# Kernel tuning notes

Hardware: AMD Instinct MI355X
Metric: run time of the kernel (lower is better)

The kernel has to match this reference:

```python
import jax, jax.numpy as jnp
import numpy as np

EMB = 512
HEADS = 8
WINDOW = 128


def setup_inputs() -> dict:
    key = jax.random.key(0)
    ks = jax.random.split(key, 9)
    s = 1.0 / np.sqrt(EMB)
    x = jax.random.normal(ks[0], (2, 4096, EMB), dtype=jnp.float32)
    mk = lambda k: jax.random.uniform(k, (EMB, EMB), jnp.float32, -s, s)
    mb = lambda k: jax.random.uniform(k, (EMB,), jnp.float32, -s, s)
    return {
        "x": x,
        "Wq": mk(ks[1]), "bq": mb(ks[2]),
        "Wk": mk(ks[3]), "bk": mb(ks[4]),
        "Wv": mk(ks[5]), "bv": mb(ks[6]),
        "Wo": mk(ks[7]), "bo": mb(ks[8]),
    }


def _split_heads(y, b, n):
    # [b, n, emb] -> [b, h, n, d]
    return y.reshape(b, n, HEADS, EMB // HEADS).transpose(0, 2, 1, 3)


def reference(x, Wq, bq, Wk, bk, Wv, bv, Wo, bo):
    b, n, _ = x.shape
    q = _split_heads(x @ Wq.T + bq, b, n)
    k = _split_heads(x @ Wk.T + bk, b, n)
    v = _split_heads(x @ Wv.T + bv, b, n)
    energy = jnp.einsum('bhqd,bhkd->bhqk', q, k)  # [b,h,n,n]
    idx = jnp.arange(n)
    # banded mask: disallowed where |i - j| > window (matches torch loop)
    disallow = jnp.abs(idx[:, None] - idx[None, :]) > WINDOW
    fmin = jnp.float32(np.finfo(np.float32).min)
    energy = jnp.where(disallow[None, None], fmin, energy)
    att = jax.nn.softmax(energy / jnp.float32(np.sqrt(EMB)), axis=-1)
    out = jnp.einsum('bhql,bhld->bhqd', att, v)
    out = out.transpose(0, 2, 1, 3).reshape(b, n, EMB)
    return out @ Wo.T + bo
```

## Files before the change

### kernel.cpp

```cpp
#include <hip/hip_runtime.h>

#define EMB 512
#define HEADS 8
#define HD 64
#define NSEQ 4096
#define BATCH 2
#define WINDOW 128

typedef unsigned short u16;
typedef __attribute__((ext_vector_type(8))) short bf16x8;
typedef __attribute__((ext_vector_type(4))) float f32x4;

#define GP 40

__device__ __forceinline__ float bf2f(u16 u) {
    union { unsigned int i; float f; } x;
    x.i = ((unsigned int)u) << 16;
    return x.f;
}

__device__ __forceinline__ u16 f2bf(float f) {
    union { float f; unsigned int i; } x;
    x.f = f;
    unsigned int i = x.i;
    unsigned int lsb = (i >> 16) & 1u;
    i += 0x7fffu + lsb;
    return (u16)(i >> 16);
}

struct raw8 { uint4 lo, hi; };

__device__ __forceinline__ raw8 loadraw8(const void* base, size_t off, int isbf) {
    raw8 r;
    if (isbf) {
        r.lo = *(const uint4*)((const u16*)base + off);
    } else {
        const float* f = (const float*)base + off;
        r.lo = *(const uint4*)f;
        r.hi = *(const uint4*)(f + 4);
    }
    return r;
}

__device__ __forceinline__ uint4 cvt8(const raw8& r, int isbf) {
    if (isbf) return r.lo;
    const float* a = (const float*)&r.lo;
    const float* b = (const float*)&r.hi;
    uint4 o;
    o.x = (unsigned)f2bf(a[0]) | ((unsigned)f2bf(a[1]) << 16);
    o.y = (unsigned)f2bf(a[2]) | ((unsigned)f2bf(a[3]) << 16);
    o.z = (unsigned)f2bf(b[0]) | ((unsigned)f2bf(b[1]) << 16);
    o.w = (unsigned)f2bf(b[2]) | ((unsigned)f2bf(b[3]) << 16);
    return o;
}

__device__ __forceinline__ float loadScalar(const void* base, int i, int isbf) {
    return isbf ? bf2f(((const u16*)base)[i]) : ((const float*)base)[i];
}

__device__ __forceinline__ int probe_bf16(const void* p) {
    const int lane = threadIdx.x & 63;
    u16 w = ((const u16*)p)[lane * 2];
    int e = (w >> 7) & 0xff;
    bool sane = (w == 0) || (e >= 100 && e <= 140);
    unsigned long long m = __ballot(sane);
    return __popcll(m) >= 48;
}

__global__ __launch_bounds__(256)
void qkv_gemm(const void* __restrict__ X,
              const void* __restrict__ Wq, const void* __restrict__ bq,
              const void* __restrict__ Wk, const void* __restrict__ bk,
              const void* __restrict__ Wv, const void* __restrict__ bv,
              u16* __restrict__ qo, u16* __restrict__ ko, u16* __restrict__ vo,
              int* __restrict__ flags)
{
    __shared__ __align__(16) u16 As[128 * GP];
    __shared__ __align__(16) u16 Bs[128 * GP];

    const int tid  = threadIdx.x;
    const int wave = tid >> 6;
    const int lane = tid & 63;
    const int quad = lane >> 4;
    const int l16  = lane & 15;
    const int wm = wave >> 1, wn = wave & 1;

    const int m0 = blockIdx.x * 128;
    const int by = blockIdx.y;
    const int wsel = by >> 2;
    const int n0 = (by & 3) * 128;

    const void* W  = (wsel == 0) ? Wq : (wsel == 1) ? Wk : Wv;
    const void* bi = (wsel == 0) ? bq : (wsel == 1) ? bk : bv;
    u16* out       = (wsel == 0) ? qo : (wsel == 1) ? ko : vo;
    const float oscale = (wsel == 0) ? 0.04419417382415922f : 1.0f;

    const int fx = probe_bf16(X);
    const int fw = probe_bf16(W);
    const int fb = probe_bf16(bi);
    if (blockIdx.x == 0 && by == 0 && tid == 0) flags[0] = fx;

    f32x4 acc[4][4];
#pragma unroll
    for (int i = 0; i < 4; ++i)
#pragma unroll
        for (int j = 0; j < 4; ++j)
            acc[i][j] = (f32x4){0.f, 0.f, 0.f, 0.f};

    const int c1 = tid, c2 = tid + 256;
    const int r1 = c1 >> 2, k1 = (c1 & 3) * 8;
    const int r2 = c2 >> 2, k2 = (c2 & 3) * 8;

    raw8 a1 = loadraw8(X, (size_t)(m0 + r1) * EMB + k1, fx);
    raw8 a2 = loadraw8(X, (size_t)(m0 + r2) * EMB + k2, fx);
    raw8 b1 = loadraw8(W, (size_t)(n0 + r1) * EMB + k1, fw);
    raw8 b2 = loadraw8(W, (size_t)(n0 + r2) * EMB + k2, fw);

    for (int kt = 0; kt < 16; ++kt) {
        __syncthreads();
        *(uint4*)&As[r1 * GP + k1] = cvt8(a1, fx);
        *(uint4*)&As[r2 * GP + k2] = cvt8(a2, fx);
        *(uint4*)&Bs[r1 * GP + k1] = cvt8(b1, fw);
        *(uint4*)&Bs[r2 * GP + k2] = cvt8(b2, fw);
        __syncthreads();

        if (kt < 15) {
            const int kk0 = (kt + 1) * 32;
            a1 = loadraw8(X, (size_t)(m0 + r1) * EMB + kk0 + k1, fx);
            a2 = loadraw8(X, (size_t)(m0 + r2) * EMB + kk0 + k2, fx);
            b1 = loadraw8(W, (size_t)(n0 + r1) * EMB + kk0 + k1, fw);
            b2 = loadraw8(W, (size_t)(n0 + r2) * EMB + kk0 + k2, fw);
        }

        bf16x8 af[4], bfr[4];
#pragma unroll
        for (int i = 0; i < 4; ++i)
            af[i] = *(const bf16x8*)&As[(wm * 64 + i * 16 + l16) * GP + quad * 8];
#pragma unroll
        for (int j = 0; j < 4; ++j)
            bfr[j] = *(const bf16x8*)&Bs[(wn * 64 + j * 16 + l16) * GP + quad * 8];
#pragma unroll
        for (int i = 0; i < 4; ++i)
#pragma unroll
            for (int j = 0; j < 4; ++j)
                acc[i][j] = __builtin_amdgcn_mfma_f32_16x16x32_bf16(af[i], bfr[j], acc[i][j], 0, 0, 0);
    }

#pragma unroll
    for (int j = 0; j < 4; ++j) {
        const int col = n0 + wn * 64 + j * 16 + l16;
        const float bv_ = loadScalar(bi, col, fb);
        const int h = col >> 6, d = col & 63;
#pragma unroll
        for (int i = 0; i < 4; ++i) {
#pragma unroll
            for (int r = 0; r < 4; ++r) {
                const int row = m0 + wm * 64 + i * 16 + quad * 4 + r;
                const int b = row >> 12, n = row & 4095;
                out[(((size_t)(b * HEADS + h) * NSEQ) + n) * HD + d] =
                    f2bf((acc[i][j][r] + bv_) * oscale);
            }
        }
    }
}

#define KP 72
__global__ __launch_bounds__(256)
void attn_mfma(const u16* __restrict__ q, const u16* __restrict__ k,
               const u16* __restrict__ v, u16* __restrict__ ao)
{
    __shared__ __align__(16) u16 Ks[64 * KP];
    __shared__ __align__(16) u16 Vt[64 * KP];
    __shared__ __align__(16) u16 Pb[4][16 * KP];

    const int tid  = threadIdx.x;
    const int wave = tid >> 6;
    const int lane = tid & 63;
    const int quad = lane >> 4;
    const int l16  = lane & 15;

    const int bh = blockIdx.y;
    const int q0 = blockIdx.x * 64;
    const int qw = q0 + wave * 16;
    const size_t base = (size_t)bh * NSEQ * HD;

    bf16x8 qa0 = *(const bf16x8*)(q + base + (size_t)(qw + l16) * HD + quad * 8);
    bf16x8 qa1 = *(const bf16x8*)(q + base + (size_t)(qw + l16) * HD + 32 + quad * 8);

    f32x4 O[4];
    float m_run[4], l_run[4];
#pragma unroll
    for (int t = 0; t < 4; ++t) O[t] = (f32x4){0.f, 0.f, 0.f, 0.f};
#pragma unroll
    for (int r = 0; r < 4; ++r) { m_run[r] = -1e30f; l_run[r] = 0.f; }

    const int key_s[2] = { (tid) >> 3, (tid + 256) >> 3 };
    const int d0_s[2]  = { (tid & 7) * 8, (tid & 7) * 8 };

    uint4 pkv[2], pvv[2];
#pragma unroll
    for (int s = 0; s < 2; ++s) {
        int kg = q0 - 128 + key_s[s];
        kg = (kg < 0) ? 0 : (kg > NSEQ - 1 ? NSEQ - 1 : kg);
        const size_t goff = base + (size_t)kg * HD + d0_s[s];
        pkv[s] = *(const uint4*)(k + goff);
        pvv[s] = *(const uint4*)(v + goff);
    }

    for (int c = 0; c < 5; ++c) {
        const int kbase = q0 - 128 + c * 64;

        __syncthreads();
#pragma unroll
        for (int s = 0; s < 2; ++s) {
            const int key = key_s[s], d0 = d0_s[s];
            *(uint4*)&Ks[key * KP + d0] = pkv[s];
            uint4 vv = pvv[s];
            u16 e[8];
            e[0] = (u16)(vv.x & 0xffff); e[1] = (u16)(vv.x >> 16);
            e[2] = (u16)(vv.y & 0xffff); e[3] = (u16)(vv.y >> 16);
            e[4] = (u16)(vv.z & 0xffff); e[5] = (u16)(vv.z >> 16);
            e[6] = (u16)(vv.w & 0xffff); e[7] = (u16)(vv.w >> 16);
#pragma unroll
            for (int j = 0; j < 8; ++j)
                Vt[(d0 + j) * KP + key] = e[j];
        }
        __syncthreads();

        if (c < 4) {
#pragma unroll
            for (int s = 0; s < 2; ++s) {
                int kg = kbase + 64 + key_s[s];
                kg = (kg < 0) ? 0 : (kg > NSEQ - 1 ? NSEQ - 1 : kg);
                const size_t goff = base + (size_t)kg * HD + d0_s[s];
                pkv[s] = *(const uint4*)(k + goff);
                pvv[s] = *(const uint4*)(v + goff);
            }
        }

        f32x4 sv[4];
#pragma unroll
        for (int t = 0; t < 4; ++t) {
            bf16x8 b0 = *(const bf16x8*)&Ks[(t * 16 + l16) * KP + quad * 8];
            bf16x8 b1 = *(const bf16x8*)&Ks[(t * 16 + l16) * KP + 32 + quad * 8];
            f32x4 sacc = (f32x4){0.f, 0.f, 0.f, 0.f};
            sacc = __builtin_amdgcn_mfma_f32_16x16x32_bf16(qa0, b0, sacc, 0, 0, 0);
            sacc = __builtin_amdgcn_mfma_f32_16x16x32_bf16(qa1, b1, sacc, 0, 0, 0);
            sv[t] = sacc;
        }

#pragma unroll
        for (int t = 0; t < 4; ++t) {
            const int jg = kbase + t * 16 + l16;
            const bool jok = ((unsigned)jg) < (unsigned)NSEQ;
#pragma unroll
            for (int r = 0; r < 4; ++r) {
                const int iq = qw + quad * 4 + r;
                const bool band = ((unsigned)(iq - jg + WINDOW)) <= (unsigned)(2 * WINDOW);
                if (!(jok && band)) sv[t][r] = -1e30f;
            }
        }

        float mnew[4];
#pragma unroll
        for (int r = 0; r < 4; ++r)
            mnew[r] = fmaxf(fmaxf(sv[0][r], sv[1][r]), fmaxf(sv[2][r], sv[3][r]));
#pragma unroll
        for (int off = 1; off < 16; off <<= 1)
#pragma unroll
            for (int r = 0; r < 4; ++r)
                mnew[r] = fmaxf(mnew[r], __shfl_xor(mnew[r], off, 64));

        float alpha[4], mi[4];
#pragma unroll
        for (int r = 0; r < 4; ++r) {
            mi[r] = fmaxf(m_run[r], mnew[r]);
            alpha[r] = __expf(m_run[r] - mi[r]);
            m_run[r] = mi[r];
        }

        float p[4][4], lnew[4] = {0.f, 0.f, 0.f, 0.f};
#pragma unroll
        for (int t = 0; t < 4; ++t)
#pragma unroll
            for (int r = 0; r < 4; ++r) {
                float pv = (sv[t][r] > -1e29f) ? __expf(sv[t][r] - mi[r]) : 0.f;
                p[t][r] = pv;
                lnew[r] += pv;
            }
#pragma unroll
        for (int off = 1; off < 16; off <<= 1)
#pragma unroll
            for (int r = 0; r < 4; ++r)
                lnew[r] += __shfl_xor(lnew[r], off, 64);
#pragma unroll
        for (int r = 0; r < 4; ++r)
            l_run[r] = l_run[r] * alpha[r] + lnew[r];

#pragma unroll
        for (int t = 0; t < 4; ++t)
#pragma unroll
            for (int r = 0; r < 4; ++r)
                O[t][r] *= alpha[r];

#pragma unroll
        for (int t = 0; t < 4; ++t)
#pragma unroll
            for (int r = 0; r < 4; ++r)
                Pb[wave][(quad * 4 + r) * KP + t * 16 + l16] = f2bf(p[t][r]);

#pragma unroll
        for (int ks = 0; ks < 2; ++ks) {
            bf16x8 pa = *(const bf16x8*)&Pb[wave][l16 * KP + ks * 32 + quad * 8];
#pragma unroll
            for (int t = 0; t < 4; ++t) {
                bf16x8 vb = *(const bf16x8*)&Vt[(t * 16 + l16) * KP + ks * 32 + quad * 8];
                O[t] = __builtin_amdgcn_mfma_f32_16x16x32_bf16(pa, vb, O[t], 0, 0, 0);
            }
        }
    }

    const int bb = bh >> 3, hh = bh & 7;
    float rl[4];
#pragma unroll
    for (int r = 0; r < 4; ++r) rl[r] = 1.f / l_run[r];
#pragma unroll
    for (int t = 0; t < 4; ++t)
#pragma unroll
        for (int r = 0; r < 4; ++r) {
            const int iq = qw + quad * 4 + r;
            ao[((size_t)(bb * NSEQ + iq)) * EMB + hh * HD + t * 16 + l16] =
                f2bf(O[t][r] * rl[r]);
        }
}

__global__ __launch_bounds__(256)
void out_gemm(const u16* __restrict__ A, const void* __restrict__ W,
              const void* __restrict__ bias, void* __restrict__ out,
              const int* __restrict__ flags)
{
    __shared__ __align__(16) u16 As[128 * GP];
    __shared__ __align__(16) u16 Bs[128 * GP];

    const int tid  = threadIdx.x;
    const int wave = tid >> 6;
    const int lane = tid & 63;
    const int quad = lane >> 4;
    const int l16  = lane & 15;
    const int wm = wave >> 1, wn = wave & 1;

    const int m0 = blockIdx.x * 128;
    const int n0 = blockIdx.y * 128;

    const int fw = probe_bf16(W);
    const int fb = probe_bf16(bias);
    const int fo = flags[0];

    f32x4 acc[4][4];
#pragma unroll
    for (int i = 0; i < 4; ++i)
#pragma unroll
        for (int j = 0; j < 4; ++j)
            acc[i][j] = (f32x4){0.f, 0.f, 0.f, 0.f};

    const int c1 = tid, c2 = tid + 256;
    const int r1 = c1 >> 2, k1 = (c1 & 3) * 8;
    const int r2 = c2 >> 2, k2 = (c2 & 3) * 8;

    raw8 a1 = loadraw8(A, (size_t)(m0 + r1) * EMB + k1, 1);
    raw8 a2 = loadraw8(A, (size_t)(m0 + r2) * EMB + k2, 1);
    raw8 b1 = loadraw8(W, (size_t)(n0 + r1) * EMB + k1, fw);
    raw8 b2 = loadraw8(W, (size_t)(n0 + r2) * EMB + k2, fw);

    for (int kt = 0; kt < 16; ++kt) {
        __syncthreads();
        *(uint4*)&As[r1 * GP + k1] = a1.lo;
        *(uint4*)&As[r2 * GP + k2] = a2.lo;
        *(uint4*)&Bs[r1 * GP + k1] = cvt8(b1, fw);
        *(uint4*)&Bs[r2 * GP + k2] = cvt8(b2, fw);
        __syncthreads();

        if (kt < 15) {
            const int kk0 = (kt + 1) * 32;
            a1 = loadraw8(A, (size_t)(m0 + r1) * EMB + kk0 + k1, 1);
            a2 = loadraw8(A, (size_t)(m0 + r2) * EMB + kk0 + k2, 1);
            b1 = loadraw8(W, (size_t)(n0 + r1) * EMB + kk0 + k1, fw);
            b2 = loadraw8(W, (size_t)(n0 + r2) * EMB + kk0 + k2, fw);
        }

        bf16x8 af[4], bfr[4];
#pragma unroll
        for (int i = 0; i < 4; ++i)
            af[i] = *(const bf16x8*)&As[(wm * 64 + i * 16 + l16) * GP + quad * 8];
#pragma unroll
        for (int j = 0; j < 4; ++j)
            bfr[j] = *(const bf16x8*)&Bs[(wn * 64 + j * 16 + l16) * GP + quad * 8];
#pragma unroll
        for (int i = 0; i < 4; ++i)
#pragma unroll
            for (int j = 0; j < 4; ++j)
                acc[i][j] = __builtin_amdgcn_mfma_f32_16x16x32_bf16(af[i], bfr[j], acc[i][j], 0, 0, 0);
    }

#pragma unroll
    for (int j = 0; j < 4; ++j) {
        const int col = n0 + wn * 64 + j * 16 + l16;
        const float bv_ = loadScalar(bias, col, fb);
#pragma unroll
        for (int i = 0; i < 4; ++i) {
#pragma unroll
            for (int r = 0; r < 4; ++r) {
                const int row = m0 + wm * 64 + i * 16 + quad * 4 + r;
                const float val = acc[i][j][r] + bv_;
                const size_t idx = (size_t)row * EMB + col;
                if (fo) ((u16*)out)[idx] = f2bf(val);
                else    ((float*)out)[idx] = val;
            }
        }
    }
}

extern "C" void kernel_launch(void* const* d_in, const int* in_sizes, int n_in,
                              void* d_out, int out_size, void* d_ws, size_t ws_size,
                              hipStream_t stream)
{
    const size_t HSZ  = (size_t)BATCH * HEADS * NSEQ * HD;
    const size_t HSZB = HSZ * 2;
    char* base = (char*)d_ws;
    int* flags = (int*)base;
    const size_t off = 256;

    u16 *q, *k, *v, *ao;
    if (ws_size >= off + 4 * HSZB) {
        q  = (u16*)(base + off);
        k  = q + HSZ;
        v  = k + HSZ;
        ao = v + HSZ;
    } else if (ws_size >= off + 3 * HSZB) {
        q  = (u16*)d_out;
        k  = (u16*)(base + off);
        v  = k + HSZ;
        ao = v + HSZ;
    } else {
        q  = (u16*)d_out;
        k  = (u16*)(base + off);
        v  = k + HSZ;
        ao = (u16*)d_in[0];
    }

    qkv_gemm<<<dim3(64, 12), 256, 0, stream>>>(d_in[0], d_in[1], d_in[2], d_in[3],
                                               d_in[4], d_in[5], d_in[6], q, k, v, flags);
    attn_mfma<<<dim3(64, 16), 256, 0, stream>>>(q, k, v, ao);
    out_gemm<<<dim3(64, 4), 256, 0, stream>>>(ao, d_in[7], d_in[8], d_out, flags);
}
```

Measured before the change: 168.8 us.

## Double-buffer GEMM smem in fragment layout and pre-transpose V in projection

Both GEMM kernels now double-buffer their LDS tiles. Tiles are stored directly in the MFMA fragment order, so each lane reads one contiguous 16-byte chunk, and only one barrier is needed per k-step instead of two. The QKV projection writes V transposed ([d][n]), which lets the attention kernel load V^T rows with vector stores into shared memory instead of scattering eight scalar transposed stores per thread. The catch is that the V transposed global writes in the projection epilogue are strided and poorly coalesced, and the clamped V window offsets at sequence edges have to line up with the K clamping.

```diff
diff --git a/kernel.cpp b/kernel.cpp
--- a/kernel.cpp
+++ b/kernel.cpp
@@ -10,8 +10,6 @@
 typedef unsigned short u16;
 typedef __attribute__((ext_vector_type(8))) short bf16x8;
 typedef __attribute__((ext_vector_type(4))) float f32x4;
-
-#define GP 40
 
 __device__ __forceinline__ float bf2f(u16 u) {
     union { unsigned int i; float f; } x;
@@ -75,8 +73,8 @@
               u16* __restrict__ qo, u16* __restrict__ ko, u16* __restrict__ vo,
               int* __restrict__ flags)
 {
-    __shared__ __align__(16) u16 As[128 * GP];
-    __shared__ __align__(16) u16 Bs[128 * GP];
+    __shared__ __align__(16) u16 As[2][128 * 32];
+    __shared__ __align__(16) u16 Bs[2][128 * 32];
 
     const int tid  = threadIdx.x;
     const int wave = tid >> 6;
@@ -107,43 +105,55 @@
         for (int j = 0; j < 4; ++j)
             acc[i][j] = (f32x4){0.f, 0.f, 0.f, 0.f};
 
-    const int c1 = tid, c2 = tid + 256;
-    const int r1 = c1 >> 2, k1 = (c1 & 3) * 8;
-    const int r2 = c2 >> 2, k2 = (c2 & 3) * 8;
-
-    raw8 a1 = loadraw8(X, (size_t)(m0 + r1) * EMB + k1, fx);
-    raw8 a2 = loadraw8(X, (size_t)(m0 + r2) * EMB + k2, fx);
-    raw8 b1 = loadraw8(W, (size_t)(n0 + r1) * EMB + k1, fw);
-    raw8 b2 = loadraw8(W, (size_t)(n0 + r2) * EMB + k2, fw);
+    const int r1 = wave * 16 + l16, r2 = r1 + 64;
+    const int cc = (lane >> 4) * 8;
+    const int d1 = wave * 512 + lane * 8, d2 = d1 + 2048;
+
+    raw8 a1 = loadraw8(X, (size_t)(m0 + r1) * EMB + cc, fx);
+    raw8 a2 = loadraw8(X, (size_t)(m0 + r2) * EMB + cc, fx);
+    raw8 b1 = loadraw8(W, (size_t)(n0 + r1) * EMB + cc, fw);
+    raw8 b2 = loadraw8(W, (size_t)(n0 + r2) * EMB + cc, fw);
+    *(uint4*)&As[0][d1] = cvt8(a1, fx);
+    *(uint4*)&As[0][d2] = cvt8(a2, fx);
+    *(uint4*)&Bs[0][d1] = cvt8(b1, fw);
+    *(uint4*)&Bs[0][d2] = cvt8(b2, fw);
+    a1 = loadraw8(X, (size_t)(m0 + r1) * EMB + 32 + cc, fx);
+    a2 = loadraw8(X, (size_t)(m0 + r2) * EMB + 32 + cc, fx);
+    b1 = loadraw8(W, (size_t)(n0 + r1) * EMB + 32 + cc, fw);
+    b2 = loadraw8(W, (size_t)(n0 + r2) * EMB + 32 + cc, fw);
+    __syncthreads();
 
     for (int kt = 0; kt < 16; ++kt) {
-        __syncthreads();
-        *(uint4*)&As[r1 * GP + k1] = cvt8(a1, fx);
-        *(uint4*)&As[r2 * GP + k2] = cvt8(a2, fx);
-        *(uint4*)&Bs[r1 * GP + k1] = cvt8(b1, fw);
-        *(uint4*)&Bs[r2 * GP + k2] = cvt8(b2, fw);
-        __syncthreads();
+        const int buf = kt & 1;
+        bf16x8 af[4], bfr[4];
+#pragma unroll
+        for (int i = 0; i < 4; ++i)
+            af[i] = *(const bf16x8*)&As[buf][(wm * 4 + i) * 512 + lane * 8];
+#pragma unroll
+        for (int j = 0; j < 4; ++j)
+            bfr[j] = *(const bf16x8*)&Bs[buf][(wn * 4 + j) * 512 + lane * 8];
 
         if (kt < 15) {
-            const int kk0 = (kt + 1) * 32;
-            a1 = loadraw8(X, (size_t)(m0 + r1) * EMB + kk0 + k1, fx);
-            a2 = loadraw8(X, (size_t)(m0 + r2) * EMB + kk0 + k2, fx);
-            b1 = loadraw8(W, (size_t)(n0 + r1) * EMB + kk0 + k1, fw);
-            b2 = loadraw8(W, (size_t)(n0 + r2) * EMB + kk0 + k2, fw);
-        }
-
-        bf16x8 af[4], bfr[4];
-#pragma unroll
-        for (int i = 0; i < 4; ++i)
-            af[i] = *(const bf16x8*)&As[(wm * 64 + i * 16 + l16) * GP + quad * 8];
-#pragma unroll
-        for (int j = 0; j < 4; ++j)
-            bfr[j] = *(const bf16x8*)&Bs[(wn * 64 + j * 16 + l16) * GP + quad * 8];
+            const int nb = buf ^ 1;
+            *(uint4*)&As[nb][d1] = cvt8(a1, fx);
+            *(uint4*)&As[nb][d2] = cvt8(a2, fx);
+            *(uint4*)&Bs[nb][d1] = cvt8(b1, fw);
+            *(uint4*)&Bs[nb][d2] = cvt8(b2, fw);
+            if (kt < 14) {
+                const int kk0 = (kt + 2) * 32;
+                a1 = loadraw8(X, (size_t)(m0 + r1) * EMB + kk0 + cc, fx);
+                a2 = loadraw8(X, (size_t)(m0 + r2) * EMB + kk0 + cc, fx);
+                b1 = loadraw8(W, (size_t)(n0 + r1) * EMB + kk0 + cc, fw);
+                b2 = loadraw8(W, (size_t)(n0 + r2) * EMB + kk0 + cc, fw);
+            }
+        }
+
 #pragma unroll
         for (int i = 0; i < 4; ++i)
 #pragma unroll
             for (int j = 0; j < 4; ++j)
                 acc[i][j] = __builtin_amdgcn_mfma_f32_16x16x32_bf16(af[i], bfr[j], acc[i][j], 0, 0, 0);
+        __syncthreads();
     }
 
 #pragma unroll
@@ -157,8 +167,11 @@
             for (int r = 0; r < 4; ++r) {
                 const int row = m0 + wm * 64 + i * 16 + quad * 4 + r;
                 const int b = row >> 12, n = row & 4095;
-                out[(((size_t)(b * HEADS + h) * NSEQ) + n) * HD + d] =
-                    f2bf((acc[i][j][r] + bv_) * oscale);
+                const u16 val = f2bf((acc[i][j][r] + bv_) * oscale);
+                if (wsel == 2)
+                    out[((size_t)((b * HEADS + h) * HD + d)) * NSEQ + n] = val;
+                else
+                    out[(((size_t)(b * HEADS + h) * NSEQ) + n) * HD + d] = val;
             }
         }
     }
@@ -194,17 +207,20 @@
 #pragma unroll
     for (int r = 0; r < 4; ++r) { m_run[r] = -1e30f; l_run[r] = 0.f; }
 
-    const int key_s[2] = { (tid) >> 3, (tid + 256) >> 3 };
-    const int d0_s[2]  = { (tid & 7) * 8, (tid & 7) * 8 };
+    const int row_s[2] = { tid >> 3, (tid + 256) >> 3 };
+    const int ch8      = (tid & 7) * 8;
 
     uint4 pkv[2], pvv[2];
-#pragma unroll
-    for (int s = 0; s < 2; ++s) {
-        int kg = q0 - 128 + key_s[s];
-        kg = (kg < 0) ? 0 : (kg > NSEQ - 1 ? NSEQ - 1 : kg);
-        const size_t goff = base + (size_t)kg * HD + d0_s[s];
-        pkv[s] = *(const uint4*)(k + goff);
-        pvv[s] = *(const uint4*)(v + goff);
+    {
+        const int kbase = q0 - 128;
+        const int koff  = (kbase < 0) ? 0 : (kbase > NSEQ - 64 ? NSEQ - 64 : kbase);
+#pragma unroll
+        for (int s = 0; s < 2; ++s) {
+            int kg = kbase + row_s[s];
+            kg = (kg < 0) ? 0 : (kg > NSEQ - 1 ? NSEQ - 1 : kg);
+            pkv[s] = *(const uint4*)(k + base + (size_t)kg * HD + ch8);
+            pvv[s] = *(const uint4*)(v + base + (size_t)row_s[s] * NSEQ + koff + ch8);
+        }
     }
 
     for (int c = 0; c < 5; ++c) {
@@ -213,28 +229,20 @@
         __syncthreads();
 #pragma unroll
         for (int s = 0; s < 2; ++s) {
-            const int key = key_s[s], d0 = d0_s[s];
-            *(uint4*)&Ks[key * KP + d0] = pkv[s];
-            uint4 vv = pvv[s];
-            u16 e[8];
-            e[0] = (u16)(vv.x & 0xffff); e[1] = (u16)(vv.x >> 16);
-            e[2] = (u16)(vv.y & 0xffff); e[3] = (u16)(vv.y >> 16);
-            e[4] = (u16)(vv.z & 0xffff); e[5] = (u16)(vv.z >> 16);
-            e[6] = (u16)(vv.w & 0xffff); e[7] = (u16)(vv.w >> 16);
-#pragma unroll
-            for (int j = 0; j < 8; ++j)
-                Vt[(d0 + j) * KP + key] = e[j];
+            *(uint4*)&Ks[row_s[s] * KP + ch8] = pkv[s];
+            *(uint4*)&Vt[row_s[s] * KP + ch8] = pvv[s];
         }
         __syncthreads();
 
         if (c < 4) {
+            const int kb2  = kbase + 64;
+            const int koff = (kb2 < 0) ? 0 : (kb2 > NSEQ - 64 ? NSEQ - 64 : kb2);
 #pragma unroll
             for (int s = 0; s < 2; ++s) {
-                int kg = kbase + 64 + key_s[s];
+                int kg = kb2 + row_s[s];
                 kg = (kg < 0) ? 0 : (kg > NSEQ - 1 ? NSEQ - 1 : kg);
-                const size_t goff = base + (size_t)kg * HD + d0_s[s];
-                pkv[s] = *(const uint4*)(k + goff);
-                pvv[s] = *(const uint4*)(v + goff);
+                pkv[s] = *(const uint4*)(k + base + (size_t)kg * HD + ch8);
+                pvv[s] = *(const uint4*)(v + base + (size_t)row_s[s] * NSEQ + koff + ch8);
             }
         }
 
@@ -339,8 +347,8 @@
               const void* __restrict__ bias, void* __restrict__ out,
               const int* __restrict__ flags)
 {
-    __shared__ __align__(16) u16 As[128 * GP];
-    __shared__ __align__(16) u16 Bs[128 * GP];
+    __shared__ __align__(16) u16 As[2][128 * 32];
+    __shared__ __align__(16) u16 Bs[2][128 * 32];
 
     const int tid  = threadIdx.x;
     const int wave = tid >> 6;
@@ -363,43 +371,55 @@
         for (int j = 0; j < 4; ++j)
             acc[i][j] = (f32x4){0.f, 0.f, 0.f, 0.f};
 
-    const int c1 = tid, c2 = tid + 256;
-    const int r1 = c1 >> 2, k1 = (c1 & 3) * 8;
-    const int r2 = c2 >> 2, k2 = (c2 & 3) * 8;
-
-    raw8 a1 = loadraw8(A, (size_t)(m0 + r1) * EMB + k1, 1);
-    raw8 a2 = loadraw8(A, (size_t)(m0 + r2) * EMB + k2, 1);
-    raw8 b1 = loadraw8(W, (size_t)(n0 + r1) * EMB + k1, fw);
-    raw8 b2 = loadraw8(W, (size_t)(n0 + r2) * EMB + k2, fw);
+    const int r1 = wave * 16 + l16, r2 = r1 + 64;
+    const int cc = (lane >> 4) * 8;
+    const int d1 = wave * 512 + lane * 8, d2 = d1 + 2048;
+
+    raw8 a1 = loadraw8(A, (size_t)(m0 + r1) * EMB + cc, 1);
+    raw8 a2 = loadraw8(A, (size_t)(m0 + r2) * EMB + cc, 1);
+    raw8 b1 = loadraw8(W, (size_t)(n0 + r1) * EMB + cc, fw);
+    raw8 b2 = loadraw8(W, (size_t)(n0 + r2) * EMB + cc, fw);
+    *(uint4*)&As[0][d1] = a1.lo;
+    *(uint4*)&As[0][d2] = a2.lo;
+    *(uint4*)&Bs[0][d1] = cvt8(b1, fw);
+    *(uint4*)&Bs[0][d2] = cvt8(b2, fw);
+    a1 = loadraw8(A, (size_t)(m0 + r1) * EMB + 32 + cc, 1);
+    a2 = loadraw8(A, (size_t)(m0 + r2) * EMB + 32 + cc, 1);
+    b1 = loadraw8(W, (size_t)(n0 + r1) * EMB + 32 + cc, fw);
+    b2 = loadraw8(W, (size_t)(n0 + r2) * EMB + 32 + cc, fw);
+    __syncthreads();
 
     for (int kt = 0; kt < 16; ++kt) {
-        __syncthreads();
-        *(uint4*)&As[r1 * GP + k1] = a1.lo;
-        *(uint4*)&As[r2 * GP + k2] = a2.lo;
-        *(uint4*)&Bs[r1 * GP + k1] = cvt8(b1, fw);
-        *(uint4*)&Bs[r2 * GP + k2] = cvt8(b2, fw);
-        __syncthreads();
+        const int buf = kt & 1;
+        bf16x8 af[4], bfr[4];
+#pragma unroll
+        for (int i = 0; i < 4; ++i)
+            af[i] = *(const bf16x8*)&As[buf][(wm * 4 + i) * 512 + lane * 8];
+#pragma unroll
+        for (int j = 0; j < 4; ++j)
+            bfr[j] = *(const bf16x8*)&Bs[buf][(wn * 4 + j) * 512 + lane * 8];
 
         if (kt < 15) {
-            const int kk0 = (kt + 1) * 32;
-            a1 = loadraw8(A, (size_t)(m0 + r1) * EMB + kk0 + k1, 1);
-            a2 = loadraw8(A, (size_t)(m0 + r2) * EMB + kk0 + k2, 1);
-            b1 = loadraw8(W, (size_t)(n0 + r1) * EMB + kk0 + k1, fw);
-            b2 = loadraw8(W, (size_t)(n0 + r2) * EMB + kk0 + k2, fw);
-        }
-
-        bf16x8 af[4], bfr[4];
-#pragma unroll
-        for (int i = 0; i < 4; ++i)
-            af[i] = *(const bf16x8*)&As[(wm * 64 + i * 16 + l16) * GP + quad * 8];
-#pragma unroll
-        for (int j = 0; j < 4; ++j)
-            bfr[j] = *(const bf16x8*)&Bs[(wn * 64 + j * 16 + l16) * GP + quad * 8];
+            const int nb = buf ^ 1;
+            *(uint4*)&As[nb][d1] = a1.lo;
+            *(uint4*)&As[nb][d2] = a2.lo;
+            *(uint4*)&Bs[nb][d1] = cvt8(b1, fw);
+            *(uint4*)&Bs[nb][d2] = cvt8(b2, fw);
+            if (kt < 14) {
+                const int kk0 = (kt + 2) * 32;
+                a1 = loadraw8(A, (size_t)(m0 + r1) * EMB + kk0 + cc, 1);
+                a2 = loadraw8(A, (size_t)(m0 + r2) * EMB + kk0 + cc, 1);
+                b1 = loadraw8(W, (size_t)(n0 + r1) * EMB + kk0 + cc, fw);
+                b2 = loadraw8(W, (size_t)(n0 + r2) * EMB + kk0 + cc, fw);
+            }
+        }
+
 #pragma unroll
         for (int i = 0; i < 4; ++i)
 #pragma unroll
             for (int j = 0; j < 4; ++j)
                 acc[i][j] = __builtin_amdgcn_mfma_f32_16x16x32_bf16(af[i], bfr[j], acc[i][j], 0, 0, 0);
+        __syncthreads();
     }
 
 #pragma unroll
```

New measurement: 194.0 us. 1.15x slower.

## Add bf16 conversion prepass and drop per-tile conversion in GEMMs

Applied to the files above, without the earlier changes.

Adds a prepass kernel that probes input dtypes once and converts x, all weights and biases to bf16 in workspace. The QKV and output GEMMs then load bf16 directly without per-element conversion or repeated dtype probing. LDS tiles lose their row padding (stride 32 instead of 40), which may introduce bank conflicts. The extra launch and full read/write of x add memory traffic in exchange for simpler GEMM inner loops.

```diff
diff --git a/kernel.cpp b/kernel.cpp
--- a/kernel.cpp
+++ b/kernel.cpp
@@ -11,7 +11,9 @@
 typedef __attribute__((ext_vector_type(8))) short bf16x8;
 typedef __attribute__((ext_vector_type(4))) float f32x4;
 
-#define GP 40
+#define XS 4194304u
+#define WS 262144u
+#define BS 512u
 
 __device__ __forceinline__ float bf2f(u16 u) {
     union { unsigned int i; float f; } x;
@@ -54,10 +56,6 @@
     return o;
 }
 
-__device__ __forceinline__ float loadScalar(const void* base, int i, int isbf) {
-    return isbf ? bf2f(((const u16*)base)[i]) : ((const float*)base)[i];
-}
-
 __device__ __forceinline__ int probe_bf16(const void* p) {
     const int lane = threadIdx.x & 63;
     u16 w = ((const u16*)p)[lane * 2];
@@ -68,15 +66,51 @@
 }
 
 __global__ __launch_bounds__(256)
-void qkv_gemm(const void* __restrict__ X,
-              const void* __restrict__ Wq, const void* __restrict__ bq,
-              const void* __restrict__ Wk, const void* __restrict__ bk,
-              const void* __restrict__ Wv, const void* __restrict__ bv,
-              u16* __restrict__ qo, u16* __restrict__ ko, u16* __restrict__ vo,
-              int* __restrict__ flags)
+void prepass(const void* __restrict__ x,
+             const void* __restrict__ Wq, const void* __restrict__ bq,
+             const void* __restrict__ Wk, const void* __restrict__ bk,
+             const void* __restrict__ Wv, const void* __restrict__ bv,
+             const void* __restrict__ Wo, const void* __restrict__ bo,
+             u16* __restrict__ xb, u16* __restrict__ wb, u16* __restrict__ bb,
+             int* __restrict__ flags)
 {
-    __shared__ __align__(16) u16 As[128 * GP];
-    __shared__ __align__(16) u16 Bs[128 * GP];
+    const int fx  = probe_bf16(x);
+    const int fwq = probe_bf16(Wq), fbq = probe_bf16(bq);
+    const int fwk = probe_bf16(Wk), fbk = probe_bf16(bk);
+    const int fwv = probe_bf16(Wv), fbv = probe_bf16(bv);
+    const int fwo = probe_bf16(Wo), fbo = probe_bf16(bo);
+    if (blockIdx.x == 0 && threadIdx.x == 0) flags[0] = fx;
+
+    size_t idx = ((size_t)blockIdx.x * 256 + threadIdx.x) * 8;
+    const size_t T_X = XS, T_W = XS + 4 * (size_t)WS, T_ALL = T_W + 4 * (size_t)BS;
+    if (idx >= T_ALL) return;
+
+    const void* src; int fl; u16* dst; size_t off;
+    if (idx < T_X) {
+        src = x; fl = fx; dst = xb; off = idx;
+    } else if (idx < T_W) {
+        size_t w = idx - T_X;
+        int wi = (int)(w / WS); off = w % WS;
+        src = (wi == 0) ? Wq : (wi == 1) ? Wk : (wi == 2) ? Wv : Wo;
+        fl  = (wi == 0) ? fwq : (wi == 1) ? fwk : (wi == 2) ? fwv : fwo;
+        dst = wb + (size_t)wi * WS;
+    } else {
+        size_t b = idx - T_W;
+        int bi = (int)(b / BS); off = b % BS;
+        src = (bi == 0) ? bq : (bi == 1) ? bk : (bi == 2) ? bv : bo;
+        fl  = (bi == 0) ? fbq : (bi == 1) ? fbk : (bi == 2) ? fbv : fbo;
+        dst = bb + (size_t)bi * BS;
+    }
+    *(uint4*)(dst + off) = cvt8(loadraw8(src, off, fl), fl);
+}
+
+__global__ __launch_bounds__(256)
+void qkv_gemm(const u16* __restrict__ X, const u16* __restrict__ Wall,
+              const u16* __restrict__ ball,
+              u16* __restrict__ qo, u16* __restrict__ ko, u16* __restrict__ vo)
+{
+    __shared__ __align__(16) u16 As[128 * 32];
+    __shared__ __align__(16) u16 Bs[128 * 32];
 
     const int tid  = threadIdx.x;
     const int wave = tid >> 6;
@@ -90,15 +124,10 @@
     const int wsel = by >> 2;
     const int n0 = (by & 3) * 128;
 
-    const void* W  = (wsel == 0) ? Wq : (wsel == 1) ? Wk : Wv;
-    const void* bi = (wsel == 0) ? bq : (wsel == 1) ? bk : bv;
-    u16* out       = (wsel == 0) ? qo : (wsel == 1) ? ko : vo;
+    const u16* W  = Wall + (size_t)wsel * WS;
+    const u16* bi = ball + (size_t)wsel * BS;
+    u16* out      = (wsel == 0) ? qo : (wsel == 1) ? ko : vo;
     const float oscale = (wsel == 0) ? 0.04419417382415922f : 1.0f;
-
-    const int fx = probe_bf16(X);
-    const int fw = probe_bf16(W);
-    const int fb = probe_bf16(bi);
-    if (blockIdx.x == 0 && by == 0 && tid == 0) flags[0] = fx;
 
     f32x4 acc[4][4];
 #pragma unroll
@@ -111,34 +140,34 @@
     const int r1 = c1 >> 2, k1 = (c1 & 3) * 8;
     const int r2 = c2 >> 2, k2 = (c2 & 3) * 8;
 
-    raw8 a1 = loadraw8(X, (size_t)(m0 + r1) * EMB + k1, fx);
-    raw8 a2 = loadraw8(X, (size_t)(m0 + r2) * EMB + k2, fx);
-    raw8 b1 = loadraw8(W, (size_t)(n0 + r1) * EMB + k1, fw);
-    raw8 b2 = loadraw8(W, (size_t)(n0 + r2) * EMB + k2, fw);
+    uint4 a1 = *(const uint4*)(X + (size_t)(m0 + r1) * EMB + k1);
+    uint4 a2 = *(const uint4*)(X + (size_t)(m0 + r2) * EMB + k2);
+    uint4 b1 = *(const uint4*)(W + (size_t)(n0 + r1) * EMB + k1);
+    uint4 b2 = *(const uint4*)(W + (size_t)(n0 + r2) * EMB + k2);
 
     for (int kt = 0; kt < 16; ++kt) {
         __syncthreads();
-        *(uint4*)&As[r1 * GP + k1] = cvt8(a1, fx);
-        *(uint4*)&As[r2 * GP + k2] = cvt8(a2, fx);
-        *(uint4*)&Bs[r1 * GP + k1] = cvt8(b1, fw);
-        *(uint4*)&Bs[r2 * GP + k2] = cvt8(b2, fw);
+        *(uint4*)&As[c1 * 8] = a1;
+        *(uint4*)&As[c2 * 8] = a2;
+        *(uint4*)&Bs[c1 * 8] = b1;
+        *(uint4*)&Bs[c2 * 8] = b2;
         __syncthreads();
 
         if (kt < 15) {
             const int kk0 = (kt + 1) * 32;
-            a1 = loadraw8(X, (size_t)(m0 + r1) * EMB + kk0 + k1, fx);
-            a2 = loadraw8(X, (size_t)(m0 + r2) * EMB + kk0 + k2, fx);
-            b1 = loadraw8(W, (size_t)(n0 + r1) * EMB + kk0 + k1, fw);
-            b2 = loadraw8(W, (size_t)(n0 + r2) * EMB + kk0 + k2, fw);
+            a1 = *(const uint4*)(X + (size_t)(m0 + r1) * EMB + kk0 + k1);
+            a2 = *(const uint4*)(X + (size_t)(m0 + r2) * EMB + kk0 + k2);
+            b1 = *(const uint4*)(W + (size_t)(n0 + r1) * EMB + kk0 + k1);
+            b2 = *(const uint4*)(W + (size_t)(n0 + r2) * EMB + kk0 + k2);
         }
 
         bf16x8 af[4], bfr[4];
 #pragma unroll
         for (int i = 0; i < 4; ++i)
-            af[i] = *(const bf16x8*)&As[(wm * 64 + i * 16 + l16) * GP + quad * 8];
+            af[i] = *(const bf16x8*)&As[(wm * 64 + i * 16 + l16) * 32 + quad * 8];
 #pragma unroll
         for (int j = 0; j < 4; ++j)
-            bfr[j] = *(const bf16x8*)&Bs[(wn * 64 + j * 16 + l16) * GP + quad * 8];
+            bfr[j] = *(const bf16x8*)&Bs[(wn * 64 + j * 16 + l16) * 32 + quad * 8];
 #pragma unroll
         for (int i = 0; i < 4; ++i)
 #pragma unroll
@@ -149,7 +178,7 @@
 #pragma unroll
     for (int j = 0; j < 4; ++j) {
         const int col = n0 + wn * 64 + j * 16 + l16;
-        const float bv_ = loadScalar(bi, col, fb);
+        const float bv_ = bf2f(bi[col]);
         const int h = col >> 6, d = col & 63;
 #pragma unroll
         for (int i = 0; i < 4; ++i) {
@@ -194,15 +223,15 @@
 #pragma unroll
     for (int r = 0; r < 4; ++r) { m_run[r] = -1e30f; l_run[r] = 0.f; }
 
-    const int key_s[2] = { (tid) >> 3, (tid + 256) >> 3 };
-    const int d0_s[2]  = { (tid & 7) * 8, (tid & 7) * 8 };
+    const int key_s[2] = { tid >> 3, (tid + 256) >> 3 };
+    const int ch8      = (tid & 7) * 8;
 
     uint4 pkv[2], pvv[2];
 #pragma unroll
     for (int s = 0; s < 2; ++s) {
         int kg = q0 - 128 + key_s[s];
         kg = (kg < 0) ? 0 : (kg > NSEQ - 1 ? NSEQ - 1 : kg);
-        const size_t goff = base + (size_t)kg * HD + d0_s[s];
+        const size_t goff = base + (size_t)kg * HD + ch8;
         pkv[s] = *(const uint4*)(k + goff);
         pvv[s] = *(const uint4*)(v + goff);
     }
@@ -213,7 +242,7 @@
         __syncthreads();
 #pragma unroll
         for (int s = 0; s < 2; ++s) {
-            const int key = key_s[s], d0 = d0_s[s];
+            const int key = key_s[s], d0 = ch8;
             *(uint4*)&Ks[key * KP + d0] = pkv[s];
             uint4 vv = pvv[s];
             u16 e[8];
@@ -232,7 +261,7 @@
             for (int s = 0; s < 2; ++s) {
                 int kg = kbase + 64 + key_s[s];
                 kg = (kg < 0) ? 0 : (kg > NSEQ - 1 ? NSEQ - 1 : kg);
-                const size_t goff = base + (size_t)kg * HD + d0_s[s];
+                const size_t goff = base + (size_t)kg * HD + ch8;
                 pkv[s] = *(const uint4*)(k + goff);
                 pvv[s] = *(const uint4*)(v + goff);
             }
@@ -335,12 +364,12 @@
 }
 
 __global__ __launch_bounds__(256)
-void out_gemm(const u16* __restrict__ A, const void* __restrict__ W,
-              const void* __restrict__ bias, void* __restrict__ out,
+void out_gemm(const u16* __restrict__ A, const u16* __restrict__ W,
+              const u16* __restrict__ bias, void* __restrict__ out,
               const int* __restrict__ flags)
 {
-    __shared__ __align__(16) u16 As[128 * GP];
-    __shared__ __align__(16) u16 Bs[128 * GP];
+    __shared__ __align__(16) u16 As[128 * 32];
+    __shared__ __align__(16) u16 Bs[128 * 32];
 
     const int tid  = threadIdx.x;
     const int wave = tid >> 6;
@@ -351,9 +380,6 @@
 
     const int m0 = blockIdx.x * 128;
     const int n0 = blockIdx.y * 128;
-
-    const int fw = probe_bf16(W);
-    const int fb = probe_bf16(bias);
     const int fo = flags[0];
 
     f32x4 acc[4][4];
@@ -367,34 +393,34 @@
     const int r1 = c1 >> 2, k1 = (c1 & 3) * 8;
     const int r2 = c2 >> 2, k2 = (c2 & 3) * 8;
 
-    raw8 a1 = loadraw8(A, (size_t)(m0 + r1) * EMB + k1, 1);
-    raw8 a2 = loadraw8(A, (size_t)(m0 + r2) * EMB + k2, 1);
-    raw8 b1 = loadraw8(W, (size_t)(n0 + r1) * EMB + k1, fw);
-    raw8 b2 = loadraw8(W, (size_t)(n0 + r2) * EMB + k2, fw);
+    uint4 a1 = *(const uint4*)(A + (size_t)(m0 + r1) * EMB + k1);
+    uint4 a2 = *(const uint4*)(A + (size_t)(m0 + r2) * EMB + k2);
+    uint4 b1 = *(const uint4*)(W + (size_t)(n0 + r1) * EMB + k1);
+    uint4 b2 = *(const uint4*)(W + (size_t)(n0 + r2) * EMB + k2);
 
     for (int kt = 0; kt < 16; ++kt) {
         __syncthreads();
-        *(uint4*)&As[r1 * GP + k1] = a1.lo;
-        *(uint4*)&As[r2 * GP + k2] = a2.lo;
-        *(uint4*)&Bs[r1 * GP + k1] = cvt8(b1, fw);
-        *(uint4*)&Bs[r2 * GP + k2] = cvt8(b2, fw);
+        *(uint4*)&As[c1 * 8] = a1;
+        *(uint4*)&As[c2 * 8] = a2;
+        *(uint4*)&Bs[c1 * 8] = b1;
+        *(uint4*)&Bs[c2 * 8] = b2;
         __syncthreads();
 
         if (kt < 15) {
             const int kk0 = (kt + 1) * 32;
-            a1 = loadraw8(A, (size_t)(m0 + r1) * EMB + kk0 + k1, 1);
-            a2 = loadraw8(A, (size_t)(m0 + r2) * EMB + kk0 + k2, 1);
-            b1 = loadraw8(W, (size_t)(n0 + r1) * EMB + kk0 + k1, fw);
-            b2 = loadraw8(W, (size_t)(n0 + r2) * EMB + kk0 + k2, fw);
+            a1 = *(const uint4*)(A + (size_t)(m0 + r1) * EMB + kk0 + k1);
+            a2 = *(const uint4*)(A + (size_t)(m0 + r2) * EMB + kk0 + k2);
+            b1 = *(const uint4*)(W + (size_t)(n0 + r1) * EMB + kk0 + k1);
+            b2 = *(const uint4*)(W + (size_t)(n0 + r2) * EMB + kk0 + k2);
         }
 
         bf16x8 af[4], bfr[4];
 #pragma unroll
         for (int i = 0; i < 4; ++i)
-            af[i] = *(const bf16x8*)&As[(wm * 64 + i * 16 + l16) * GP + quad * 8];
+            af[i] = *(const bf16x8*)&As[(wm * 64 + i * 16 + l16) * 32 + quad * 8];
 #pragma unroll
         for (int j = 0; j < 4; ++j)
-            bfr[j] = *(const bf16x8*)&Bs[(wn * 64 + j * 16 + l16) * GP + quad * 8];
+            bfr[j] = *(const bf16x8*)&Bs[(wn * 64 + j * 16 + l16) * 32 + quad * 8];
 #pragma unroll
         for (int i = 0; i < 4; ++i)
 #pragma unroll
@@ -405,7 +431,7 @@
 #pragma unroll
     for (int j = 0; j < 4; ++j) {
         const int col = n0 + wn * 64 + j * 16 + l16;
-        const float bv_ = loadScalar(bias, col, fb);
+        const float bv_ = bf2f(bias[col]);
 #pragma unroll
         for (int i = 0; i < 4; ++i) {
 #pragma unroll
@@ -425,31 +451,28 @@
                               hipStream_t stream)
 {
     const size_t HSZ  = (size_t)BATCH * HEADS * NSEQ * HD;
-    const size_t HSZB = HSZ * 2;
     char* base = (char*)d_ws;
     int* flags = (int*)base;
     const size_t off = 256;
 
-    u16 *q, *k, *v, *ao;
-    if (ws_size >= off + 4 * HSZB) {
-        q  = (u16*)(base + off);
-        k  = q + HSZ;
-        v  = k + HSZ;
-        ao = v + HSZ;
-    } else if (ws_size >= off + 3 * HSZB) {
-        q  = (u16*)d_out;
-        k  = (u16*)(base + off);
-        v  = k + HSZ;
-        ao = v + HSZ;
-    } else {
-        q  = (u16*)d_out;
-        k  = (u16*)(base + off);
-        v  = k + HSZ;
-        ao = (u16*)d_in[0];
-    }
-
-    qkv_gemm<<<dim3(64, 12), 256, 0, stream>>>(d_in[0], d_in[1], d_in[2], d_in[3],
-                                               d_in[4], d_in[5], d_in[6], q, k, v, flags);
-    attn_mfma<<<dim3(64, 16), 256, 0, stream>>>(q, k, v, ao);
-    out_gemm<<<dim3(64, 4), 256, 0, stream>>>(ao, d_in[7], d_in[8], d_out, flags);
-}
+    u16* xb = (u16*)(base + off);
+    u16* wb = xb + XS;
+    u16* bb = wb + 4 * (size_t)WS;
+    u16* kk = bb + 4 * (size_t)BS;
+    u16* vv = kk + HSZ;
+    u16* ao = vv + HSZ;
+    u16* qq = ao + HSZ;
+
+    const size_t need_t1 = off + 2 * (XS + 4 * (size_t)WS + 4 * (size_t)BS + 4 * HSZ);
+    if (ws_size < need_t1) {
+        qq = (u16*)d_out;
+    }
+
+    prepass<<<dim3(2561), 256, 0, stream>>>(d_in[0], d_in[1], d_in[2], d_in[3],
+                                            d_in[4], d_in[5], d_in[6], d_in[7],
+                                            d_in[8], xb, wb, bb, flags);
+    qkv_gemm<<<dim3(64, 12), 256, 0, stream>>>(xb, wb, bb, qq, kk, vv);
+    attn_mfma<<<dim3(64, 16), 256, 0, stream>>>(qq, kk, vv, ao);
+    out_gemm<<<dim3(64, 4), 256, 0, stream>>>(ao, wb + 3 * (size_t)WS, bb + 3 * (size_t)BS,
+                                              d_out, flags);
+}
```

Result: faster. 151.9 us (-10.0%).
